# Kernel optimization log

Hardware: AMD Instinct MI355X
Metric: run time of the kernel (lower is better)

## Reference

```python
import jax, jax.numpy as jnp
import numpy as np

N = 50000        # nodes
E = 1600000      # edges (before self loops)
C_IN = 128
C_OUT = 128
G = 64           # graphs in the batch
NEG_SLOPE = 0.2  # GATConv default


def setup_inputs() -> dict:
    key = jax.random.key(0)
    ks = jax.random.split(key, 12)
    u = jax.random.normal(ks[0], (N, C_IN), jnp.float32)
    edge_index = jax.random.randint(ks[1], (2, E), 0, N, dtype=jnp.int32)
    batch = jnp.sort(jax.random.randint(ks[2], (N,), 0, G, dtype=jnp.int32))
    g1 = 1.0 / np.sqrt(C_IN)
    g2 = 1.0 / np.sqrt(C_OUT)
    return {
        "u": u,
        "W1": jax.random.normal(ks[3], (C_IN, C_OUT), jnp.float32) * g1,
        "a_src1": jax.random.normal(ks[4], (C_OUT,), jnp.float32) * g2,
        "a_dst1": jax.random.normal(ks[5], (C_OUT,), jnp.float32) * g2,
        "b1": jnp.zeros((C_OUT,), jnp.float32),
        "W2": jax.random.normal(ks[6], (C_OUT, C_OUT), jnp.float32) * g2,
        "a_src2": jax.random.normal(ks[7], (C_OUT,), jnp.float32) * g2,
        "a_dst2": jax.random.normal(ks[8], (C_OUT,), jnp.float32) * g2,
        "b2": jnp.zeros((C_OUT,), jnp.float32),
        "edge_index": edge_index,
        "batch": batch,
    }


def gat_conv(x, edge_index, W, a_src, a_dst, b):
    """PyG GATConv, heads=1: linear -> edge attention -> scatter softmax -> scatter add."""
    n = x.shape[0]
    h = x @ W                                        # [N, C]
    loops = jnp.arange(n, dtype=edge_index.dtype)    # add_self_loops=True
    src = jnp.concatenate([edge_index[0], loops])    # message source j
    dst = jnp.concatenate([edge_index[1], loops])    # aggregation target i
    alpha_s = h @ a_src                              # [N]
    alpha_d = h @ a_dst                              # [N]
    e = jax.nn.leaky_relu(alpha_s[src] + alpha_d[dst], NEG_SLOPE)  # [E+N]
    m = jax.ops.segment_max(e, dst, num_segments=n)  # stable softmax per target
    w = jnp.exp(e - m[dst])
    denom = jax.ops.segment_sum(w, dst, num_segments=n)
    alpha = w / denom[dst]                           # [E+N]
    out = jax.ops.segment_sum(alpha[:, None] * h[src], dst, num_segments=n)
    return out + b


def reference(u, W1, a_src1, a_dst1, b1, W2, a_src2, a_dst2, b2, edge_index, batch):
    h = jax.nn.selu(gat_conv(u, edge_index, W1, a_src1, a_dst1, b1))
    h = jax.nn.selu(gat_conv(h, edge_index, W2, a_src2, a_dst2, b2))
    # global_mean_pool
    s = jax.ops.segment_sum(h, batch, num_segments=G)                      # [G, C]
    cnt = jax.ops.segment_sum(jnp.ones((h.shape[0],), h.dtype), batch, num_segments=G)
    return s / jnp.maximum(cnt, 1.0)[:, None]
```

## Files before the change

kernel.cpp:

```cpp
#include <hip/hip_runtime.h>
#include <hip/hip_bf16.h>
#include <math.h>

#define CH 128
#define PSHIFT 8
#define PSIZE (1 << PSHIFT)
#define CHUNK 4096
#define EPT 16
#define MAXP 256
#define PCAP 12288
#define PS 8

typedef __attribute__((ext_vector_type(8))) short short8;
typedef __attribute__((ext_vector_type(4))) float f32x4;

__device__ __forceinline__ float seluf(float x) {
    const float scale = 1.0507009873554804934193349852946f;
    const float alpha = 1.6732632423543772848170429916717f;
    return x > 0.0f ? scale * x : scale * alpha * (__expf(x) - 1.0f);
}

__device__ __forceinline__ float lrelu(float x) {
    return x > 0.0f ? x : 0.2f * x;
}

__device__ __forceinline__ short bfc(float f) {
    union { __hip_bfloat16 b; short s; } u;
    u.b = __float2bfloat16(f);
    return u.s;
}

__device__ __forceinline__ unsigned pk(float lo, float hi) {
    return ((unsigned)(unsigned short)bfc(hi) << 16) | (unsigned short)bfc(lo);
}


__global__ __launch_bounds__(256) void k_part(const int* __restrict__ ei,
                                              int* __restrict__ pfill,
                                              unsigned* __restrict__ staged,
                                              int E, int NP) {
    __shared__ int hist[MAXP];
    __shared__ int base[MAXP];
    const int tid = threadIdx.x;
    const int j0 = blockIdx.x * CHUNK;
    for (int i = tid; i < NP; i += 256) hist[i] = 0;
    __syncthreads();
    int part[EPT], rank[EPT];
    unsigned rec[EPT];
#pragma unroll
    for (int e = 0; e < EPT; ++e) {
        int j = j0 + e * 256 + tid;
        part[e] = -1;
        if (j < E) {
            int s = ei[j], d = ei[E + j];
            part[e] = d >> PSHIFT;
            rec[e] = ((unsigned)(d & (PSIZE - 1)) << 24) | (unsigned)s;
            rank[e] = atomicAdd(&hist[part[e]], 1);
        }
    }
    __syncthreads();
    for (int i = tid; i < NP; i += 256)
        base[i] = hist[i] ? atomicAdd(&pfill[i], hist[i]) : 0;
    __syncthreads();
#pragma unroll
    for (int e = 0; e < EPT; ++e)
        if (part[e] >= 0)
            staged[(size_t)part[e] * PCAP + base[part[e]] + rank[e]] = rec[e];
}


__global__ __launch_bounds__(256) void k_fat(
    const unsigned* __restrict__ staged, const int* __restrict__ pfill,
    int* __restrict__ rowptr, int* __restrict__ csr, int n, int E, int NP,
    const float* __restrict__ x, const float* __restrict__ W,
    const float* __restrict__ a_s, const float* __restrict__ a_d,
    __hip_bfloat16* __restrict__ hb, float* __restrict__ as_o,
    float* __restrict__ ad_o) {
    __shared__ __align__(16) char sm[32768];
    const int tid = threadIdx.x;

    if ((int)blockIdx.x < NP) {
        int* lcnt = (int*)sm;
        int* lrow = lcnt + PSIZE;
        int* sc   = lrow + PSIZE;
        int* psc  = sc + PSIZE;
        const int p = blockIdx.x;
        const int d0 = p << PSHIFT;
        psc[tid] = (tid < NP) ? pfill[tid] : 0;
        lcnt[tid] = 0;
        __syncthreads();
        for (int off = 1; off < 256; off <<= 1) {
            int v = (tid >= off) ? psc[tid - off] : 0;
            __syncthreads();
            psc[tid] += v;
            __syncthreads();
        }
        const int pbase = psc[p] - pfill[p];
        const size_t rbeg = (size_t)p * PCAP;
        const size_t rend = rbeg + pfill[p];
        const int rb = pbase + d0;
        for (size_t r = rbeg + tid; r < rend; r += 256)
            atomicAdd(&lcnt[staged[r] >> 24], 1);
        __syncthreads();
        int myv = (d0 + tid < n) ? lcnt[tid] + 1 : 0;
        sc[tid] = myv;
        __syncthreads();
        for (int off = 1; off < 256; off <<= 1) {
            int v = (tid >= off) ? sc[tid - off] : 0;
            __syncthreads();
            sc[tid] += v;
            __syncthreads();
        }
        if (d0 + tid < n) {
            int rp = rb + sc[tid] - myv;
            lrow[tid] = rp;
            rowptr[d0 + tid] = rp;
            csr[rp] = d0 + tid;
            lcnt[tid] = 0;
        }
        if (p == 0 && tid == 0) rowptr[n] = E + n;
        __syncthreads();
        for (size_t r = rbeg + tid; r < rend; r += 256) {
            unsigned v = staged[r];
            int dd = v >> 24, s = (int)(v & 0xFFFFFFu);
            int pos = lrow[dd] + 1 + atomicAdd(&lcnt[dd], 1);
            csr[pos] = s;
        }
        return;
    }

    short* WB = (short*)sm;
    for (int i = tid; i < CH * CH; i += 256) {
        int k = i >> 7, c = i & 127;
        int kb = k >> 5, kk = k & 31;
        int t = c >> 4;
        int ln = (c & 15) | ((kk >> 3) << 4);
        int j = kk & 7;
        WB[(((kb << 3) + t) << 9) + (ln << 3) + j] = bfc(W[i]);
    }
    __syncthreads();
    const int bid = blockIdx.x - NP;
    const int lane = tid & 63;
    const int wid = tid >> 6;
    const int l15 = lane & 15;
    const int lhi = lane >> 4;
    float asl[8], adl[8];
#pragma unroll
    for (int t = 0; t < 8; ++t) {
        asl[t] = a_s[t * 16 + l15];
        adl[t] = a_d[t * 16 + l15];
    }
#pragma unroll
    for (int s = 0; s < 2; ++s) {
        int r0 = bid * 128 + s * 64 + wid * 16;
        if (r0 >= n) break;
        int ar = r0 + l15; if (ar >= n) ar = n - 1;
        const float* xr = x + (size_t)ar * CH + lhi * 8;
        f32x4 acc[8];
#pragma unroll
        for (int t = 0; t < 8; ++t) acc[t] = (f32x4){0.f, 0.f, 0.f, 0.f};
#pragma unroll
        for (int kb = 0; kb < 4; ++kb) {
            float4 xa = *(const float4*)(xr + kb * 32);
            float4 xb = *(const float4*)(xr + kb * 32 + 4);
            short8 af;
            af[0] = bfc(xa.x); af[1] = bfc(xa.y); af[2] = bfc(xa.z); af[3] = bfc(xa.w);
            af[4] = bfc(xb.x); af[5] = bfc(xb.y); af[6] = bfc(xb.z); af[7] = bfc(xb.w);
#pragma unroll
            for (int t = 0; t < 8; ++t) {
                short8 bv = ((const short8*)WB)[(((kb << 3) + t) << 6) | lane];
                acc[t] = __builtin_amdgcn_mfma_f32_16x16x32_bf16(af, bv, acc[t], 0, 0, 0);
            }
        }
        float pa[4] = {0.f, 0.f, 0.f, 0.f}, pd[4] = {0.f, 0.f, 0.f, 0.f};
#pragma unroll
        for (int t = 0; t < 8; ++t) {
#pragma unroll
            for (int q = 0; q < 4; ++q) {
                int row = r0 + lhi * 4 + q;
                if (row < n)
                    hb[(size_t)row * CH + t * 16 + l15] = __float2bfloat16(acc[t][q]);
                pa[q] += acc[t][q] * asl[t];
                pd[q] += acc[t][q] * adl[t];
            }
        }
#pragma unroll
        for (int q = 0; q < 4; ++q) {
#pragma unroll
            for (int o = 1; o < 16; o <<= 1) {
                pa[q] += __shfl_xor(pa[q], o);
                pd[q] += __shfl_xor(pd[q], o);
            }
        }
        if (l15 == 0) {
#pragma unroll
            for (int q = 0; q < 4; ++q) {
                int row = r0 + lhi * 4 + q;
                if (row < n) { as_o[row] = pa[q]; ad_o[row] = pd[q]; }
            }
        }
    }
}


template <typename T>
__global__ __launch_bounds__(256) void k_gemm3(
    const T* __restrict__ x, const float* __restrict__ W,
    const float* __restrict__ a_s, const float* __restrict__ a_d,
    __hip_bfloat16* __restrict__ hb, float* __restrict__ as_o,
    float* __restrict__ ad_o, int n) {
    __shared__ short WB[4 * 8 * 64 * 8];
    const int tid = threadIdx.x;
    for (int i = tid; i < CH * CH; i += 256) {
        int k = i >> 7, c = i & 127;
        int kb = k >> 5, kk = k & 31;
        int t = c >> 4;
        int ln = (c & 15) | ((kk >> 3) << 4);
        int j = kk & 7;
        WB[(((kb << 3) + t) << 9) + (ln << 3) + j] = bfc(W[i]);
    }
    __syncthreads();
    const int lane = tid & 63;
    const int wid = tid >> 6;
    const int l15 = lane & 15;
    const int lhi = lane >> 4;
    float asl[8], adl[8];
#pragma unroll
    for (int t = 0; t < 8; ++t) {
        asl[t] = a_s[t * 16 + l15];
        adl[t] = a_d[t * 16 + l15];
    }
#pragma unroll
    for (int s = 0; s < 2; ++s) {
        int r0 = blockIdx.x * 128 + s * 64 + wid * 16;
        if (r0 >= n) break;
        int ar = r0 + l15; if (ar >= n) ar = n - 1;
        const T* xr = x + (size_t)ar * CH + lhi * 8;
        f32x4 acc[8];
#pragma unroll
        for (int t = 0; t < 8; ++t) acc[t] = (f32x4){0.f, 0.f, 0.f, 0.f};
#pragma unroll
        for (int kb = 0; kb < 4; ++kb) {
            short8 af;
            if constexpr (sizeof(T) == 4) {
                float4 xa = *(const float4*)(xr + kb * 32);
                float4 xb = *(const float4*)(xr + kb * 32 + 4);
                af[0] = bfc(xa.x); af[1] = bfc(xa.y); af[2] = bfc(xa.z); af[3] = bfc(xa.w);
                af[4] = bfc(xb.x); af[5] = bfc(xb.y); af[6] = bfc(xb.z); af[7] = bfc(xb.w);
            } else {
                af = *(const short8*)(xr + kb * 32);
            }
#pragma unroll
            for (int t = 0; t < 8; ++t) {
                short8 bv = ((const short8*)WB)[(((kb << 3) + t) << 6) | lane];
                acc[t] = __builtin_amdgcn_mfma_f32_16x16x32_bf16(af, bv, acc[t], 0, 0, 0);
            }
        }
        float pa[4] = {0.f, 0.f, 0.f, 0.f}, pd[4] = {0.f, 0.f, 0.f, 0.f};
#pragma unroll
        for (int t = 0; t < 8; ++t) {
#pragma unroll
            for (int q = 0; q < 4; ++q) {
                int row = r0 + lhi * 4 + q;
                if (row < n)
                    hb[(size_t)row * CH + t * 16 + l15] = __float2bfloat16(acc[t][q]);
                pa[q] += acc[t][q] * asl[t];
                pd[q] += acc[t][q] * adl[t];
            }
        }
#pragma unroll
        for (int q = 0; q < 4; ++q) {
#pragma unroll
            for (int o = 1; o < 16; o <<= 1) {
                pa[q] += __shfl_xor(pa[q], o);
                pd[q] += __shfl_xor(pd[q], o);
            }
        }
        if (l15 == 0) {
#pragma unroll
            for (int q = 0; q < 4; ++q) {
                int row = r0 + lhi * 4 + q;
                if (row < n) { as_o[row] = pa[q]; ad_o[row] = pd[q]; }
            }
        }
    }
}


__global__ __launch_bounds__(256) void k_fused_agg(
    const int* __restrict__ rowptr, const int* __restrict__ csr,
    const float* __restrict__ as_v, const float* __restrict__ ad_v,
    float* __restrict__ wedge, const __hip_bfloat16* __restrict__ hb,
    const float* __restrict__ bias, __hip_bfloat16* __restrict__ out, int n) {
    int gw = (int)((blockIdx.x * (size_t)blockDim.x + threadIdx.x) >> 6);
    int lane = threadIdx.x & 63;
    if (gw >= n) return;
    int beg = rowptr[gw], end = rowptr[gw + 1];
    int deg = end - beg;
    float adi = ad_v[gw];

    const int quarter = lane >> 4;
    const int c8 = lane & 15;
    float acc[8];
#pragma unroll
    for (int k = 0; k < 8; ++k) acc[k] = 0.f;
    float inv;

    if (deg <= 64) {
        bool valid = lane < deg;
        int src = valid ? csr[beg + lane] : 0;
        float e = valid ? lrelu(as_v[src] + adi) : -1e30f;
        float m = e;
#pragma unroll
        for (int o = 32; o > 0; o >>= 1) m = fmaxf(m, __shfl_xor(m, o));
        float w = valid ? __expf(e - m) : 0.f;
        float s = w;
#pragma unroll
        for (int o = 32; o > 0; o >>= 1) s += __shfl_xor(s, o);
        inv = 1.0f / s;
        for (int b = 0; b < deg; b += 16) {
            int i0 = b + quarter, i1 = b + 4 + quarter;
            int i2 = b + 8 + quarter, i3 = b + 12 + quarter;
            float w0 = __shfl(w, i0), w1 = __shfl(w, i1);
            float w2 = __shfl(w, i2), w3 = __shfl(w, i3);
            int s0 = __shfl(src, i0), s1 = __shfl(src, i1);
            int s2 = __shfl(src, i2), s3 = __shfl(src, i3);
            uint4 hv0 = ((const uint4*)hb)[(size_t)s0 * 16 + c8];
            uint4 hv1 = ((const uint4*)hb)[(size_t)s1 * 16 + c8];
            uint4 hv2 = ((const uint4*)hb)[(size_t)s2 * 16 + c8];
            uint4 hv3 = ((const uint4*)hb)[(size_t)s3 * 16 + c8];
            acc[0] += w0 * __uint_as_float(hv0.x << 16);
            acc[1] += w0 * __uint_as_float(hv0.x & 0xffff0000u);
            acc[2] += w0 * __uint_as_float(hv0.y << 16);
            acc[3] += w0 * __uint_as_float(hv0.y & 0xffff0000u);
            acc[4] += w0 * __uint_as_float(hv0.z << 16);
            acc[5] += w0 * __uint_as_float(hv0.z & 0xffff0000u);
            acc[6] += w0 * __uint_as_float(hv0.w << 16);
            acc[7] += w0 * __uint_as_float(hv0.w & 0xffff0000u);
            acc[0] += w1 * __uint_as_float(hv1.x << 16);
            acc[1] += w1 * __uint_as_float(hv1.x & 0xffff0000u);
            acc[2] += w1 * __uint_as_float(hv1.y << 16);
            acc[3] += w1 * __uint_as_float(hv1.y & 0xffff0000u);
            acc[4] += w1 * __uint_as_float(hv1.z << 16);
            acc[5] += w1 * __uint_as_float(hv1.z & 0xffff0000u);
            acc[6] += w1 * __uint_as_float(hv1.w << 16);
            acc[7] += w1 * __uint_as_float(hv1.w & 0xffff0000u);
            acc[0] += w2 * __uint_as_float(hv2.x << 16);
            acc[1] += w2 * __uint_as_float(hv2.x & 0xffff0000u);
            acc[2] += w2 * __uint_as_float(hv2.y << 16);
            acc[3] += w2 * __uint_as_float(hv2.y & 0xffff0000u);
            acc[4] += w2 * __uint_as_float(hv2.z << 16);
            acc[5] += w2 * __uint_as_float(hv2.z & 0xffff0000u);
            acc[6] += w2 * __uint_as_float(hv2.w << 16);
            acc[7] += w2 * __uint_as_float(hv2.w & 0xffff0000u);
            acc[0] += w3 * __uint_as_float(hv3.x << 16);
            acc[1] += w3 * __uint_as_float(hv3.x & 0xffff0000u);
            acc[2] += w3 * __uint_as_float(hv3.y << 16);
            acc[3] += w3 * __uint_as_float(hv3.y & 0xffff0000u);
            acc[4] += w3 * __uint_as_float(hv3.z << 16);
            acc[5] += w3 * __uint_as_float(hv3.z & 0xffff0000u);
            acc[6] += w3 * __uint_as_float(hv3.w << 16);
            acc[7] += w3 * __uint_as_float(hv3.w & 0xffff0000u);
        }
    } else {
        float m = -1e30f;
        for (int p = beg + lane; p < end; p += 64) {
            float e = lrelu(as_v[csr[p]] + adi);
            wedge[p] = e;
            m = fmaxf(m, e);
        }
#pragma unroll
        for (int o = 32; o > 0; o >>= 1) m = fmaxf(m, __shfl_xor(m, o));
        float s = 0.f;
        for (int p = beg + lane; p < end; p += 64) {
            float wv = __expf(wedge[p] - m);
            wedge[p] = wv;
            s += wv;
        }
#pragma unroll
        for (int o = 32; o > 0; o >>= 1) s += __shfl_xor(s, o);
        inv = 1.0f / s;
        for (int p = beg; p < end; p += 8) {
            int p0 = p + quarter, p1 = p + 4 + quarter;
            float w0 = 0.f, w1 = 0.f;
            int s0 = 0, s1 = 0;
            if (p0 < end) { w0 = wedge[p0]; s0 = csr[p0]; }
            if (p1 < end) { w1 = wedge[p1]; s1 = csr[p1]; }
            uint4 hv0 = ((const uint4*)hb)[(size_t)s0 * 16 + c8];
            uint4 hv1 = ((const uint4*)hb)[(size_t)s1 * 16 + c8];
            acc[0] += w0 * __uint_as_float(hv0.x << 16);
            acc[1] += w0 * __uint_as_float(hv0.x & 0xffff0000u);
            acc[2] += w0 * __uint_as_float(hv0.y << 16);
            acc[3] += w0 * __uint_as_float(hv0.y & 0xffff0000u);
            acc[4] += w0 * __uint_as_float(hv0.z << 16);
            acc[5] += w0 * __uint_as_float(hv0.z & 0xffff0000u);
            acc[6] += w0 * __uint_as_float(hv0.w << 16);
            acc[7] += w0 * __uint_as_float(hv0.w & 0xffff0000u);
            acc[0] += w1 * __uint_as_float(hv1.x << 16);
            acc[1] += w1 * __uint_as_float(hv1.x & 0xffff0000u);
            acc[2] += w1 * __uint_as_float(hv1.y << 16);
            acc[3] += w1 * __uint_as_float(hv1.y & 0xffff0000u);
            acc[4] += w1 * __uint_as_float(hv1.z << 16);
            acc[5] += w1 * __uint_as_float(hv1.z & 0xffff0000u);
            acc[6] += w1 * __uint_as_float(hv1.w << 16);
            acc[7] += w1 * __uint_as_float(hv1.w & 0xffff0000u);
        }
    }
#pragma unroll
    for (int k = 0; k < 8; ++k) {
        acc[k] += __shfl_xor(acc[k], 16);
        acc[k] += __shfl_xor(acc[k], 32);
    }
    if (quarter == 0) {
        const float4 bv0 = ((const float4*)bias)[c8 * 2];
        const float4 bv1 = ((const float4*)bias)[c8 * 2 + 1];
        float o0 = seluf(acc[0] * inv + bv0.x);
        float o1 = seluf(acc[1] * inv + bv0.y);
        float o2 = seluf(acc[2] * inv + bv0.z);
        float o3 = seluf(acc[3] * inv + bv0.w);
        float o4 = seluf(acc[4] * inv + bv1.x);
        float o5 = seluf(acc[5] * inv + bv1.y);
        float o6 = seluf(acc[6] * inv + bv1.z);
        float o7 = seluf(acc[7] * inv + bv1.w);
        uint4 ov;
        ov.x = pk(o0, o1);
        ov.y = pk(o2, o3);
        ov.z = pk(o4, o5);
        ov.w = pk(o6, o7);
        ((uint4*)out)[(size_t)gw * 16 + c8] = ov;
    }
}


__device__ int lower_bound_dev(const int* a, int n, int key) {
    int lo = 0, hi = n;
    while (lo < hi) {
        int mid = (lo + hi) >> 1;
        if (a[mid] < key) lo = mid + 1; else hi = mid;
    }
    return lo;
}

__global__ __launch_bounds__(1024) void k_pool(const __hip_bfloat16* __restrict__ x,
                                               const int* __restrict__ batchv,
                                               float* __restrict__ outp, int n) {
    int g = blockIdx.x;
    int lo = lower_bound_dev(batchv, n, g);
    int hi = lower_bound_dev(batchv, n, g + 1);
    int lane = threadIdx.x & 63, wv = threadIdx.x >> 6;
    float sx0 = 0.f, sy0 = 0.f, sx1 = 0.f, sy1 = 0.f;
    int i = lo + wv;
    for (; i + 16 < hi; i += 32) {
        unsigned u0 = ((const unsigned*)x)[(size_t)i * 64 + lane];
        unsigned u1 = ((const unsigned*)x)[(size_t)(i + 16) * 64 + lane];
        sx0 += __uint_as_float(u0 << 16);
        sy0 += __uint_as_float(u0 & 0xffff0000u);
        sx1 += __uint_as_float(u1 << 16);
        sy1 += __uint_as_float(u1 & 0xffff0000u);
    }
    if (i < hi) {
        unsigned u0 = ((const unsigned*)x)[(size_t)i * 64 + lane];
        sx0 += __uint_as_float(u0 << 16);
        sy0 += __uint_as_float(u0 & 0xffff0000u);
    }
    __shared__ float2 red[16][64];
    red[wv][lane] = make_float2(sx0 + sx1, sy0 + sy1);
    __syncthreads();
    if (wv == 0) {
        float ax = 0.f, ay = 0.f;
#pragma unroll
        for (int s = 0; s < 16; ++s) { ax += red[s][lane].x; ay += red[s][lane].y; }
        int cnt = hi - lo; if (cnt < 1) cnt = 1;
        float invc = 1.0f / (float)cnt;
        outp[(size_t)g * CH + 2 * lane] = ax * invc;
        outp[(size_t)g * CH + 2 * lane + 1] = ay * invc;
    }
}


extern "C" void kernel_launch(void* const* d_in, const int* in_sizes, int n_in,
                              void* d_out, int out_size, void* d_ws, size_t ws_size,
                              hipStream_t stream) {
    const float* u   = (const float*)d_in[0];
    const float* W1  = (const float*)d_in[1];
    const float* as1 = (const float*)d_in[2];
    const float* ad1 = (const float*)d_in[3];
    const float* b1  = (const float*)d_in[4];
    const float* W2  = (const float*)d_in[5];
    const float* as2 = (const float*)d_in[6];
    const float* ad2 = (const float*)d_in[7];
    const float* b2  = (const float*)d_in[8];
    const int* ei    = (const int*)d_in[9];
    const int* batchv= (const int*)d_in[10];

    const int N = in_sizes[0] / CH;
    const int E = in_sizes[9] / 2;
    const int M = E + N;
    const int NP = (N + PSIZE - 1) >> PSHIFT;
    const int G = out_size / CH;

    char* p = (char*)d_ws;
    auto alloc = [&](size_t bytes) {
        char* r = p;
        p += (bytes + 255) & ~(size_t)255;
        return r;
    };
    int*   pfill  = (int*)alloc((size_t)NP * 4);
    size_t zbytes = (size_t)(p - (char*)d_ws);
    int*   rowptr = (int*)alloc((size_t)(N + 1) * 4);
    int*   csr    = (int*)alloc((size_t)M * 4);
    float* asv    = (float*)alloc((size_t)N * 4);
    float* adv    = (float*)alloc((size_t)N * 4);
    __hip_bfloat16* hbuf = (__hip_bfloat16*)alloc((size_t)N * CH * 2);
    size_t wbytes = ((size_t)M * 4 + 255) & ~(size_t)255;
    size_t xbytes = (size_t)N * CH * 2;
    size_t sbytes = (size_t)NP * PCAP * 4;
    size_t blob   = wbytes + xbytes > sbytes ? wbytes + xbytes : sbytes;
    char*  bb     = alloc(blob);
    unsigned* staged = (unsigned*)bb;
    float* wedge  = (float*)bb;
    __hip_bfloat16* x2 = (__hip_bfloat16*)(bb + wbytes);

    hipMemsetAsync(d_ws, 0, zbytes, stream);

    const int gblocks = (N + 127) / 128;

    k_part<<<(E + CHUNK - 1) / CHUNK, 256, 0, stream>>>(ei, pfill, staged, E, NP);
    k_fat<<<NP + gblocks, 256, 0, stream>>>(staged, pfill, rowptr, csr, N, E, NP,
                                            u, W1, as1, ad1, hbuf, asv, adv);

    k_fused_agg<<<(N * 64 + 255) / 256, 256, 0, stream>>>(rowptr, csr, asv, adv, wedge, hbuf, b1, x2, N);

    k_gemm3<__hip_bfloat16><<<gblocks, 256, 0, stream>>>(x2, W2, as2, ad2, hbuf, asv, adv, N);
    k_fused_agg<<<(N * 64 + 255) / 256, 256, 0, stream>>>(rowptr, csr, asv, adv, wedge, hbuf, b2, x2, N);

    k_pool<<<G, 1024, 0, stream>>>(x2, batchv, (float*)d_out, N);
}
```

Measured before the change: 190.6 us.

## Split aggregation channels across two waves per node for more parallelism

The fused attention-aggregation kernel now uses two waves per target node, each owning half of the 128 channels, instead of one wave covering all channels. Each wave gathers 8 edges at once with 8 lanes per half-row, and the block index mapping keeps both halves of a node group in adjacent blocks so the shared source rows stay in cache. The aim is more waves in flight and more memory-level parallelism for the gathers. The cost is that the per-node softmax and index loads are computed twice, and for nodes with degree above 64 both waves read and write the shared edge-weight scratch buffer, which is a potential race.

```diff
diff --git a/kernel.cpp b/kernel.cpp
--- a/kernel.cpp
+++ b/kernel.cpp
@@ -9,7 +9,6 @@
 #define EPT 16
 #define MAXP 256
 #define PCAP 12288
-#define PS 8
 
 typedef __attribute__((ext_vector_type(8))) short short8;
 typedef __attribute__((ext_vector_type(4))) float f32x4;
@@ -292,15 +291,19 @@
     const float* __restrict__ as_v, const float* __restrict__ ad_v,
     float* __restrict__ wedge, const __hip_bfloat16* __restrict__ hb,
     const float* __restrict__ bias, __hip_bfloat16* __restrict__ out, int n) {
-    int gw = (int)((blockIdx.x * (size_t)blockDim.x + threadIdx.x) >> 6);
-    int lane = threadIdx.x & 63;
+    const int bid = blockIdx.x;
+    const int half = (bid >> 2) & 1;
+    const int g = (bid >> 3) * 4 + (bid & 3);
+    const int gw = g * 4 + (threadIdx.x >> 6);
+    const int lane = threadIdx.x & 63;
     if (gw >= n) return;
     int beg = rowptr[gw], end = rowptr[gw + 1];
     int deg = end - beg;
     float adi = ad_v[gw];
 
-    const int quarter = lane >> 4;
-    const int c8 = lane & 15;
+    const int grp = lane >> 3;
+    const int c8 = lane & 7;
+    const int hoff = half * 8;
     float acc[8];
 #pragma unroll
     for (int k = 0; k < 8; ++k) acc[k] = 0.f;
@@ -319,16 +322,12 @@
         for (int o = 32; o > 0; o >>= 1) s += __shfl_xor(s, o);
         inv = 1.0f / s;
         for (int b = 0; b < deg; b += 16) {
-            int i0 = b + quarter, i1 = b + 4 + quarter;
-            int i2 = b + 8 + quarter, i3 = b + 12 + quarter;
+            int i0 = b + grp;
+            int i1 = b + 8 + grp;
             float w0 = __shfl(w, i0), w1 = __shfl(w, i1);
-            float w2 = __shfl(w, i2), w3 = __shfl(w, i3);
             int s0 = __shfl(src, i0), s1 = __shfl(src, i1);
-            int s2 = __shfl(src, i2), s3 = __shfl(src, i3);
-            uint4 hv0 = ((const uint4*)hb)[(size_t)s0 * 16 + c8];
-            uint4 hv1 = ((const uint4*)hb)[(size_t)s1 * 16 + c8];
-            uint4 hv2 = ((const uint4*)hb)[(size_t)s2 * 16 + c8];
-            uint4 hv3 = ((const uint4*)hb)[(size_t)s3 * 16 + c8];
+            uint4 hv0 = ((const uint4*)hb)[(size_t)s0 * 16 + hoff + c8];
+            uint4 hv1 = ((const uint4*)hb)[(size_t)s1 * 16 + hoff + c8];
             acc[0] += w0 * __uint_as_float(hv0.x << 16);
             acc[1] += w0 * __uint_as_float(hv0.x & 0xffff0000u);
             acc[2] += w0 * __uint_as_float(hv0.y << 16);
@@ -345,22 +344,6 @@
             acc[5] += w1 * __uint_as_float(hv1.z & 0xffff0000u);
             acc[6] += w1 * __uint_as_float(hv1.w << 16);
             acc[7] += w1 * __uint_as_float(hv1.w & 0xffff0000u);
-            acc[0] += w2 * __uint_as_float(hv2.x << 16);
-            acc[1] += w2 * __uint_as_float(hv2.x & 0xffff0000u);
-            acc[2] += w2 * __uint_as_float(hv2.y << 16);
-            acc[3] += w2 * __uint_as_float(hv2.y & 0xffff0000u);
-            acc[4] += w2 * __uint_as_float(hv2.z << 16);
-            acc[5] += w2 * __uint_as_float(hv2.z & 0xffff0000u);
-            acc[6] += w2 * __uint_as_float(hv2.w << 16);
-            acc[7] += w2 * __uint_as_float(hv2.w & 0xffff0000u);
-            acc[0] += w3 * __uint_as_float(hv3.x << 16);
-            acc[1] += w3 * __uint_as_float(hv3.x & 0xffff0000u);
-            acc[2] += w3 * __uint_as_float(hv3.y << 16);
-            acc[3] += w3 * __uint_as_float(hv3.y & 0xffff0000u);
-            acc[4] += w3 * __uint_as_float(hv3.z << 16);
-            acc[5] += w3 * __uint_as_float(hv3.z & 0xffff0000u);
-            acc[6] += w3 * __uint_as_float(hv3.w << 16);
-            acc[7] += w3 * __uint_as_float(hv3.w & 0xffff0000u);
         }
     } else {
         float m = -1e30f;
@@ -380,14 +363,14 @@
 #pragma unroll
         for (int o = 32; o > 0; o >>= 1) s += __shfl_xor(s, o);
         inv = 1.0f / s;
-        for (int p = beg; p < end; p += 8) {
-            int p0 = p + quarter, p1 = p + 4 + quarter;
+        for (int p = beg; p < end; p += 16) {
+            int p0 = p + grp, p1 = p + 8 + grp;
             float w0 = 0.f, w1 = 0.f;
             int s0 = 0, s1 = 0;
             if (p0 < end) { w0 = wedge[p0]; s0 = csr[p0]; }
             if (p1 < end) { w1 = wedge[p1]; s1 = csr[p1]; }
-            uint4 hv0 = ((const uint4*)hb)[(size_t)s0 * 16 + c8];
-            uint4 hv1 = ((const uint4*)hb)[(size_t)s1 * 16 + c8];
+            uint4 hv0 = ((const uint4*)hb)[(size_t)s0 * 16 + hoff + c8];
+            uint4 hv1 = ((const uint4*)hb)[(size_t)s1 * 16 + hoff + c8];
             acc[0] += w0 * __uint_as_float(hv0.x << 16);
             acc[1] += w0 * __uint_as_float(hv0.x & 0xffff0000u);
             acc[2] += w0 * __uint_as_float(hv0.y << 16);
@@ -408,12 +391,13 @@
     }
 #pragma unroll
     for (int k = 0; k < 8; ++k) {
+        acc[k] += __shfl_xor(acc[k], 8);
         acc[k] += __shfl_xor(acc[k], 16);
         acc[k] += __shfl_xor(acc[k], 32);
     }
-    if (quarter == 0) {
-        const float4 bv0 = ((const float4*)bias)[c8 * 2];
-        const float4 bv1 = ((const float4*)bias)[c8 * 2 + 1];
+    if (grp == 0) {
+        const float4 bv0 = ((const float4*)bias)[half * 16 + c8 * 2];
+        const float4 bv1 = ((const float4*)bias)[half * 16 + c8 * 2 + 1];
         float o0 = seluf(acc[0] * inv + bv0.x);
         float o1 = seluf(acc[1] * inv + bv0.y);
         float o2 = seluf(acc[2] * inv + bv0.z);
@@ -427,7 +411,7 @@
         ov.y = pk(o2, o3);
         ov.z = pk(o4, o5);
         ov.w = pk(o6, o7);
-        ((uint4*)out)[(size_t)gw * 16 + c8] = ov;
+        ((uint4*)out)[(size_t)gw * 16 + hoff + c8] = ov;
     }
 }
 
@@ -524,15 +508,16 @@
     hipMemsetAsync(d_ws, 0, zbytes, stream);
 
     const int gblocks = (N + 127) / 128;
+    const int aggblocks = 2 * ((N + 3) / 4);
 
     k_part<<<(E + CHUNK - 1) / CHUNK, 256, 0, stream>>>(ei, pfill, staged, E, NP);
     k_fat<<<NP + gblocks, 256, 0, stream>>>(staged, pfill, rowptr, csr, N, E, NP,
                                             u, W1, as1, ad1, hbuf, asv, adv);
 
-    k_fused_agg<<<(N * 64 + 255) / 256, 256, 0, stream>>>(rowptr, csr, asv, adv, wedge, hbuf, b1, x2, N);
+    k_fused_agg<<<aggblocks, 256, 0, stream>>>(rowptr, csr, asv, adv, wedge, hbuf, b1, x2, N);
 
     k_gemm3<__hip_bfloat16><<<gblocks, 256, 0, stream>>>(x2, W2, as2, ad2, hbuf, asv, adv, N);
-    k_fused_agg<<<(N * 64 + 255) / 256, 256, 0, stream>>>(rowptr, csr, asv, adv, wedge, hbuf, b2, x2, N);
+    k_fused_agg<<<aggblocks, 256, 0, stream>>>(rowptr, csr, asv, adv, wedge, hbuf, b2, x2, N);
 
     k_pool<<<G, 1024, 0, stream>>>(x2, batchv, (float*)d_out, N);
 }
```

New measurement: 211.9 us. +11.2%, slower.
